# Performance work log

Hardware: AMD Instinct MI355X
Metric: run time of the kernel (lower is better)

The kernel has to match this reference:

```python
import jax, jax.numpy as jnp
import numpy as np
from jax import lax

INPLANES = 512
PLANES = 512
MID = PLANES // 4  # expansion = 4
G = 4              # patch_groups
EPS = 1e-5


def _conv(x, w, groups, pad):
    return lax.conv_general_dilated(
        x, w, window_strides=(1, 1), padding=[(pad, pad), (pad, pad)],
        dimension_numbers=('NCHW', 'OIHW', 'NCHW'), feature_group_count=groups)


def _bn(x, gamma, beta, mean, var):
    scale = gamma / jnp.sqrt(var + EPS)
    return x * scale[None, :, None, None] + (beta - mean * scale)[None, :, None, None]


def _upmask(mask, c, h, w):
    # [b,g,mh,mw] -> repeat each group over c//g channels (group-major channel order),
    # then nearest-upsample to (h, w) (exact integer repeat, matches F.interpolate nearest)
    b, g, mh, mw = mask.shape
    m = jnp.repeat(mask, c // g, axis=1)
    m = jnp.repeat(m, h // mh, axis=2)
    m = jnp.repeat(m, w // mw, axis=3)
    return m


def setup_inputs() -> dict:
    key = jax.random.key(0)
    ks = jax.random.split(key, 20)
    x = jax.random.normal(ks[0], (16, INPLANES, 56, 56), dtype=jnp.float32)
    mask = jax.random.randint(ks[1], (16, G, 7, 7), 0, 2).astype(jnp.float32)
    s = 0.05
    w1 = jax.random.normal(ks[2], (MID, INPLANES // G, 1, 1), dtype=jnp.float32) * s
    w2 = jax.random.normal(ks[3], (MID, MID // G, 3, 3), dtype=jnp.float32) * s
    w3 = jax.random.normal(ks[4], (PLANES, MID // G, 1, 1), dtype=jnp.float32) * s
    def bnp(k, c):
        k1, k2, k3, k4 = jax.random.split(k, 4)
        return (jax.random.normal(k1, (c,), jnp.float32) * 0.1 + 1.0,  # gamma
                jax.random.normal(k2, (c,), jnp.float32) * 0.1,        # beta
                jax.random.normal(k3, (c,), jnp.float32) * 0.1,        # running mean
                jax.random.uniform(k4, (c,), jnp.float32, 0.5, 1.5))   # running var
    g1, b1, m1, v1 = bnp(ks[5], MID)
    g2, b2, m2, v2 = bnp(ks[6], MID)
    g3, b3, m3, v3 = bnp(ks[7], PLANES)
    return dict(x=x, mask=mask, w1=w1, g1=g1, b1=b1, m1=m1, v1=v1,
                w2=w2, g2=g2, b2=b2, m2=m2, v2=v2,
                w3=w3, g3=g3, b3=b3, m3=m3, v3=v3)


def reference(x, mask, w1, g1, b1, m1, v1, w2, g2, b2, m2, v2, w3, g3, b3, m3, v3):
    b, c, h, w = x.shape
    residual = x
    mask1 = _upmask(mask, c, h, w)           # [b, c, h, w]
    out = x * mask1
    out = jax.nn.relu(_bn(_conv(out, w1, G, 0), g1, b1, m1, v1))  # [b, MID, h, w]
    mask2 = _upmask(mask, out.shape[1], h, w)
    out = out * mask2
    out = jax.nn.relu(_bn(_conv(out, w2, G, 1), g2, b2, m2, v2))
    out = out * mask2
    out = _bn(_conv(out, w3, G, 0), g3, b3, m3, v3)
    out = out + residual
    return jax.nn.relu(out)
```

## Files before the change

### kernel.cpp

```cpp
#include <hip/hip_runtime.h>
#include <stdint.h>

typedef unsigned short U16;
typedef unsigned int   U32;
typedef __attribute__((ext_vector_type(8))) short short8;
typedef __attribute__((ext_vector_type(4))) float floatx4;

#define HW 3136

__device__ __forceinline__ U16 f2b(float f){
    union { float f; unsigned int i; } v; v.f = f;
    unsigned int u = (v.i + 0x7FFFu + ((v.i >> 16) & 1u)) >> 16;
    return (U16)u;
}
__device__ __forceinline__ short8 pack8(const float* p){
    float4 a = *reinterpret_cast<const float4*>(p);
    float4 b = *reinterpret_cast<const float4*>(p + 4);
    short8 r;
    r[0]=(short)f2b(a.x); r[1]=(short)f2b(a.y); r[2]=(short)f2b(a.z); r[3]=(short)f2b(a.w);
    r[4]=(short)f2b(b.x); r[5]=(short)f2b(b.y); r[6]=(short)f2b(b.z); r[7]=(short)f2b(b.w);
    return r;
}

__global__ void k_pre(const float* __restrict__ w2,
                      const float* g1, const float* b1, const float* m1, const float* v1,
                      const float* g2, const float* b2, const float* m2, const float* v2,
                      const float* g3, const float* b3, const float* m3, const float* v3,
                      U16* __restrict__ w2t, float* __restrict__ bn){
  int i = blockIdx.x * 256 + threadIdx.x;
  if (i < 4*9*32*32) {
    int ic  = i & 31;
    int oc  = (i >> 5) & 31;
    int gt  = i >> 10;
    int g_  = gt / 9, tap = gt % 9;
    w2t[i] = f2b(w2[((g_*32 + oc)*32 + ic)*9 + tap]);
  } else {
    int j = i - 4*9*32*32;
    if (j >= 768) return;
    const float *gp, *bp, *mp, *vp; int c, so, sho;
    if (j < 128)      { c = j;       gp=g1; bp=b1; mp=m1; vp=v1; so = 0;   sho = 128;  }
    else if (j < 256) { c = j - 128; gp=g2; bp=b2; mp=m2; vp=v2; so = 256; sho = 384;  }
    else              { c = j - 256; gp=g3; bp=b3; mp=m3; vp=v3; so = 512; sho = 1024; }
    float s = gp[c] / sqrtf(vp[c] + 1e-5f);
    bn[so + c]  = s;
    bn[sho + c] = bp[c] - mp[c] * s;
  }
}

__global__ __launch_bounds__(512) void k_conv1(const float* __restrict__ x,
        const float* __restrict__ mask, const float* __restrict__ w1,
        const float* __restrict__ bn, U16* __restrict__ t1){
  const int t = threadIdx.x;
  const int lane = t & 63, wave = t >> 6;
  const int quad = lane >> 4, l15 = lane & 15;
  const int oct = wave & 1, pxq = wave >> 1;
  const int b = blockIdx.z, g = blockIdx.y, mh = blockIdx.x;
  const int h0 = mh*8, wbase = pxq*112;
  __shared__ float mk[7];
  __shared__ __align__(16) U16 xs[32*456];
  if (t < 7) mk[t] = mask[((b*4 + g)*7 + mh)*7 + t];
  const float* xg = x + (size_t)(b*512 + g*128)*HW + h0*56;
  U16* t1g = t1 + (size_t)(b*128 + g*32)*HW + h0*56;

  const float* wg = w1 + (size_t)(g*32)*128;
  short8 afr[4];
  #pragma unroll
  for (int ks = 0; ks < 4; ++ks)
    afr[ks] = pack8(wg + (oct*16 + l15)*128 + ks*32 + quad*8);

  floatx4 acc[7] = {};
  #pragma unroll
  for (int ch = 0; ch < 4; ++ch){
    __syncthreads();
    #pragma unroll
    for (int k = 0; k < 7; ++k){
      int idx = k*512 + t;
      int ic = idx / 112, f = idx - ic*112;
      int px = f*4;
      float4 v = *reinterpret_cast<const float4*>(xg + (size_t)(ch*32 + ic)*HW + px);
      float m = mk[(px % 56) >> 3];
      U32 lo = (U32)f2b(v.x*m) | ((U32)f2b(v.y*m) << 16);
      U32 hi = (U32)f2b(v.z*m) | ((U32)f2b(v.w*m) << 16);
      *reinterpret_cast<uint2*>(&xs[ic*456 + px]) = make_uint2(lo, hi);
    }
    __syncthreads();
    #pragma unroll
    for (int pxt = 0; pxt < 7; ++pxt){
      short8 bfr;
      #pragma unroll
      for (int j = 0; j < 8; ++j)
        bfr[j] = (short)xs[(quad*8 + j)*456 + wbase + pxt*16 + l15];
      acc[pxt] = __builtin_amdgcn_mfma_f32_16x16x32_bf16(afr[ch], bfr, acc[pxt], 0,0,0);
    }
  }
  #pragma unroll
  for (int reg = 0; reg < 4; ++reg){
    int oc = oct*16 + quad*4 + reg;
    float sc = bn[g*32 + oc], sh = bn[128 + g*32 + oc];
    #pragma unroll
    for (int pxt = 0; pxt < 7; ++pxt){
      int px = wbase + pxt*16 + l15;
      float y = fmaxf(sc*acc[pxt][reg] + sh, 0.0f) * mk[(px % 56) >> 3];
      t1g[(size_t)oc*HW + px] = f2b(y);
    }
  }
}

__global__ __launch_bounds__(512) void k_conv23(const U16* __restrict__ t1,
        const float* __restrict__ mask, const U16* __restrict__ w2t,
        const float* __restrict__ w3, const float* __restrict__ bn,
        const float* __restrict__ x, float* __restrict__ out){
  const int t = threadIdx.x;
  const int lane = t & 63, wave = t >> 6;
  const int quad = lane >> 4, l15 = lane & 15;
  const int b = blockIdx.z, g = blockIdx.y, mh = blockIdx.x;
  const int h0 = mh*8;
  __shared__ float mk[7];
  __shared__ __align__(16) U16 s[32*720];
  __shared__ __align__(16) U16 t2s[32*456];
  if (t < 7) mk[t] = mask[((b*4 + g)*7 + mh)*7 + t];
  if (t < 320){
    int ic = t / 10, r = t - ic*10;
    s[(ic*10 + r)*72 + 7]  = 0;
    s[(ic*10 + r)*72 + 64] = 0;
  }
  const U16* tg = t1 + (size_t)(b*128 + g*32)*HW;
  #pragma unroll
  for (int k = 0; k < 5; ++k){
    int idx = k*512 + t;
    if (idx < 2240){
      int ic = idx / 70, rem = idx - ic*70;
      int r = rem / 7, seg = rem - r*7;
      int hh = h0 - 1 + r;
      uint4 v = make_uint4(0,0,0,0);
      if (hh >= 0 && hh < 56)
        v = *reinterpret_cast<const uint4*>(tg + (size_t)ic*HW + hh*56 + seg*8);
      *reinterpret_cast<uint4*>(&s[(ic*10 + r)*72 + 8 + seg*8]) = v;
    }
  }
  __syncthreads();

  {
    const int oct = wave & 1, rq = wave >> 1;
    const U16* wg = w2t + g*9*32*32;
    floatx4 acc[7] = {};
    #pragma unroll
    for (int kh = 0; kh < 3; ++kh){
      const int lr = rq*2 + (l15 >> 3) + kh;
      #pragma unroll
      for (int kw = 0; kw < 3; ++kw){
        int tap = kh*3 + kw;
        short8 a0 = *reinterpret_cast<const short8*>(wg + (tap*32 + oct*16 + l15)*32 + quad*8);
        #pragma unroll
        for (int pxt = 0; pxt < 7; ++pxt){
          int lc = 7 + pxt*8 + (l15 & 7) + kw;
          short8 bfr;
          #pragma unroll
          for (int j = 0; j < 8; ++j)
            bfr[j] = (short)s[((quad*8 + j)*10 + lr)*72 + lc];
          acc[pxt] = __builtin_amdgcn_mfma_f32_16x16x32_bf16(a0, bfr, acc[pxt], 0,0,0);
        }
      }
    }
    const int pr = rq*2 + (l15 >> 3);
    #pragma unroll
    for (int reg = 0; reg < 4; ++reg){
      int oc = oct*16 + quad*4 + reg;
      float sc = bn[256 + g*32 + oc], sh = bn[384 + g*32 + oc];
      #pragma unroll
      for (int pxt = 0; pxt < 7; ++pxt){
        float y = fmaxf(sc*acc[pxt][reg] + sh, 0.0f) * mk[pxt];
        t2s[oc*456 + pr*56 + pxt*8 + (l15 & 7)] = f2b(y);
      }
    }
  }
  __syncthreads();

  {
    short8 afr = pack8(w3 + (size_t)(g*128 + wave*16 + l15)*32 + quad*8);
    const float* scp = bn + 512 + g*128 + wave*16 + quad*4;
    const float* shp = bn + 1024 + g*128 + wave*16 + quad*4;
    const float* xg = x + (size_t)(b*512 + g*128)*HW + h0*56;
    float* og = out + (size_t)(b*512 + g*128)*HW + h0*56;
    #pragma unroll
    for (int tt = 0; tt < 28; ++tt){
      short8 bfr;
      #pragma unroll
      for (int j = 0; j < 8; ++j)
        bfr[j] = (short)t2s[(quad*8 + j)*456 + tt*16 + l15];
      floatx4 acc = {};
      acc = __builtin_amdgcn_mfma_f32_16x16x32_bf16(afr, bfr, acc, 0,0,0);
      int px = tt*16 + l15;
      #pragma unroll
      for (int reg = 0; reg < 4; ++reg){
        size_t o2 = (size_t)(wave*16 + quad*4 + reg)*HW + px;
        og[o2] = fmaxf(scp[reg]*acc[reg] + shp[reg] + xg[o2], 0.0f);
      }
    }
  }
}

extern "C" void kernel_launch(void* const* d_in, const int* in_sizes, int n_in,
                              void* d_out, int out_size, void* d_ws, size_t ws_size,
                              hipStream_t stream){
  const float* x    = (const float*)d_in[0];
  const float* mask = (const float*)d_in[1];
  const float* w1   = (const float*)d_in[2];
  const float* g1   = (const float*)d_in[3];
  const float* b1   = (const float*)d_in[4];
  const float* m1   = (const float*)d_in[5];
  const float* v1   = (const float*)d_in[6];
  const float* w2   = (const float*)d_in[7];
  const float* g2   = (const float*)d_in[8];
  const float* b2   = (const float*)d_in[9];
  const float* m2   = (const float*)d_in[10];
  const float* v2   = (const float*)d_in[11];
  const float* w3   = (const float*)d_in[12];
  const float* g3   = (const float*)d_in[13];
  const float* b3   = (const float*)d_in[14];
  const float* m3   = (const float*)d_in[15];
  const float* v3   = (const float*)d_in[16];

  char* ws = (char*)d_ws;
  U16*   w2t = (U16*)ws;
  float* bn  = (float*)(ws + 73728);
  U16*   t1  = (U16*)(ws + 79872);

  k_pre<<<147, 256, 0, stream>>>(w2, g1,b1,m1,v1, g2,b2,m2,v2, g3,b3,m3,v3, w2t, bn);
  dim3 grid(7, 4, 16);
  k_conv1<<<grid, 512, 0, stream>>>(x, mask, w1, bn, t1);
  k_conv23<<<grid, 512, 0, stream>>>(t1, mask, w2t, w3, bn, x, (float*)d_out);
}
```

Measured before the change: 287.0 us.

## Store intermediates channel-last so MFMA B-fragments load as single vectors

Changes the intermediate t1 from channel-major to pixel-major [b,g,px,32] layout and rearranges the conv2 and conv3 LDS tiles with 32 channels contiguous per pixel (padded stride 40). The B operand of each MFMA can then be read as one 16-byte vector instead of eight scalar LDS loads. The conv2 input buffer is reused for the t2 tile, which needs an extra barrier but lowers LDS use. The conv1 LDS row stride is padded from 456 to 460 to reduce bank conflicts, and the conv1 epilogue writes 4 packed channels per store.

```diff
diff --git a/kernel.cpp b/kernel.cpp
--- a/kernel.cpp
+++ b/kernel.cpp
@@ -7,6 +7,7 @@
 typedef __attribute__((ext_vector_type(4))) float floatx4;
 
 #define HW 3136
+#define ICS 40
 
 __device__ __forceinline__ U16 f2b(float f){
     union { float f; unsigned int i; } v; v.f = f;
@@ -57,10 +58,10 @@
   const int b = blockIdx.z, g = blockIdx.y, mh = blockIdx.x;
   const int h0 = mh*8, wbase = pxq*112;
   __shared__ float mk[7];
-  __shared__ __align__(16) U16 xs[32*456];
+  __shared__ __align__(16) U16 xs[32*460];
   if (t < 7) mk[t] = mask[((b*4 + g)*7 + mh)*7 + t];
   const float* xg = x + (size_t)(b*512 + g*128)*HW + h0*56;
-  U16* t1g = t1 + (size_t)(b*128 + g*32)*HW + h0*56;
+  U16* t1g = t1 + ((size_t)(b*4 + g)*HW + h0*56)*32;
 
   const float* wg = w1 + (size_t)(g*32)*128;
   short8 afr[4];
@@ -81,7 +82,7 @@
       float m = mk[(px % 56) >> 3];
       U32 lo = (U32)f2b(v.x*m) | ((U32)f2b(v.y*m) << 16);
       U32 hi = (U32)f2b(v.z*m) | ((U32)f2b(v.w*m) << 16);
-      *reinterpret_cast<uint2*>(&xs[ic*456 + px]) = make_uint2(lo, hi);
+      *reinterpret_cast<uint2*>(&xs[ic*460 + px]) = make_uint2(lo, hi);
     }
     __syncthreads();
     #pragma unroll
@@ -89,20 +90,22 @@
       short8 bfr;
       #pragma unroll
       for (int j = 0; j < 8; ++j)
-        bfr[j] = (short)xs[(quad*8 + j)*456 + wbase + pxt*16 + l15];
+        bfr[j] = (short)xs[(quad*8 + j)*460 + wbase + pxt*16 + l15];
       acc[pxt] = __builtin_amdgcn_mfma_f32_16x16x32_bf16(afr[ch], bfr, acc[pxt], 0,0,0);
     }
   }
-  #pragma unroll
-  for (int reg = 0; reg < 4; ++reg){
-    int oc = oct*16 + quad*4 + reg;
-    float sc = bn[g*32 + oc], sh = bn[128 + g*32 + oc];
-    #pragma unroll
-    for (int pxt = 0; pxt < 7; ++pxt){
-      int px = wbase + pxt*16 + l15;
-      float y = fmaxf(sc*acc[pxt][reg] + sh, 0.0f) * mk[(px % 56) >> 3];
-      t1g[(size_t)oc*HW + px] = f2b(y);
-    }
+  const float* scp = bn + g*32 + oct*16 + quad*4;
+  const float* shp = scp + 128;
+  #pragma unroll
+  for (int pxt = 0; pxt < 7; ++pxt){
+    int px = wbase + pxt*16 + l15;
+    float m = mk[(px % 56) >> 3];
+    U16 y[4];
+    #pragma unroll
+    for (int reg = 0; reg < 4; ++reg)
+      y[reg] = f2b(fmaxf(scp[reg]*acc[pxt][reg] + shp[reg], 0.0f) * m);
+    *reinterpret_cast<uint2*>(t1g + (size_t)px*32 + oct*16 + quad*4) =
+        make_uint2((U32)y[0] | ((U32)y[1]<<16), (U32)y[2] | ((U32)y[3]<<16));
   }
 }
 
@@ -116,34 +119,35 @@
   const int b = blockIdx.z, g = blockIdx.y, mh = blockIdx.x;
   const int h0 = mh*8;
   __shared__ float mk[7];
-  __shared__ __align__(16) U16 s[32*720];
-  __shared__ __align__(16) U16 t2s[32*456];
+  __shared__ __align__(16) U16 s[580*ICS];
+  U16* t2s = s;
   if (t < 7) mk[t] = mask[((b*4 + g)*7 + mh)*7 + t];
-  if (t < 320){
-    int ic = t / 10, r = t - ic*10;
-    s[(ic*10 + r)*72 + 7]  = 0;
-    s[(ic*10 + r)*72 + 64] = 0;
-  }
-  const U16* tg = t1 + (size_t)(b*128 + g*32)*HW;
+  if (t < 80){
+    int si = t >> 2, part = t & 3;
+    int r = si >> 1, side = si & 1;
+    *reinterpret_cast<uint4*>(&s[(r*58 + (side ? 57 : 0))*ICS + part*8]) =
+        make_uint4(0,0,0,0);
+  }
+  const U16* tg = t1 + (size_t)(b*4 + g)*HW*32;
   #pragma unroll
   for (int k = 0; k < 5; ++k){
     int idx = k*512 + t;
     if (idx < 2240){
-      int ic = idx / 70, rem = idx - ic*70;
-      int r = rem / 7, seg = rem - r*7;
+      int part = idx & 3, pxi = idx >> 2;
+      int r = pxi / 56, c = pxi - r*56;
       int hh = h0 - 1 + r;
       uint4 v = make_uint4(0,0,0,0);
-      if (hh >= 0 && hh < 56)
-        v = *reinterpret_cast<const uint4*>(tg + (size_t)ic*HW + hh*56 + seg*8);
-      *reinterpret_cast<uint4*>(&s[(ic*10 + r)*72 + 8 + seg*8]) = v;
+      if ((unsigned)hh < 56u)
+        v = *reinterpret_cast<const uint4*>(tg + (size_t)(hh*56 + c)*32 + part*8);
+      *reinterpret_cast<uint4*>(&s[(r*58 + c + 1)*ICS + part*8]) = v;
     }
   }
   __syncthreads();
 
+  const int oct = wave & 1, rq = wave >> 1;
+  floatx4 acc[7] = {};
   {
-    const int oct = wave & 1, rq = wave >> 1;
     const U16* wg = w2t + g*9*32*32;
-    floatx4 acc[7] = {};
     #pragma unroll
     for (int kh = 0; kh < 3; ++kh){
       const int lr = rq*2 + (l15 >> 3) + kh;
@@ -153,25 +157,30 @@
         short8 a0 = *reinterpret_cast<const short8*>(wg + (tap*32 + oct*16 + l15)*32 + quad*8);
         #pragma unroll
         for (int pxt = 0; pxt < 7; ++pxt){
-          int lc = 7 + pxt*8 + (l15 & 7) + kw;
-          short8 bfr;
-          #pragma unroll
-          for (int j = 0; j < 8; ++j)
-            bfr[j] = (short)s[((quad*8 + j)*10 + lr)*72 + lc];
+          int cslot = pxt*8 + (l15 & 7) + kw;
+          short8 bfr = *reinterpret_cast<const short8*>(
+              &s[(lr*58 + cslot)*ICS + quad*8]);
           acc[pxt] = __builtin_amdgcn_mfma_f32_16x16x32_bf16(a0, bfr, acc[pxt], 0,0,0);
         }
       }
     }
+  }
+  __syncthreads();
+
+  {
     const int pr = rq*2 + (l15 >> 3);
-    #pragma unroll
-    for (int reg = 0; reg < 4; ++reg){
-      int oc = oct*16 + quad*4 + reg;
-      float sc = bn[256 + g*32 + oc], sh = bn[384 + g*32 + oc];
-      #pragma unroll
-      for (int pxt = 0; pxt < 7; ++pxt){
-        float y = fmaxf(sc*acc[pxt][reg] + sh, 0.0f) * mk[pxt];
-        t2s[oc*456 + pr*56 + pxt*8 + (l15 & 7)] = f2b(y);
-      }
+    const float* scp = bn + 256 + g*32 + oct*16 + quad*4;
+    const float* shp = bn + 384 + g*32 + oct*16 + quad*4;
+    #pragma unroll
+    for (int pxt = 0; pxt < 7; ++pxt){
+      float m = mk[pxt];
+      U16 y[4];
+      #pragma unroll
+      for (int reg = 0; reg < 4; ++reg)
+        y[reg] = f2b(fmaxf(scp[reg]*acc[pxt][reg] + shp[reg], 0.0f) * m);
+      int px = pr*56 + pxt*8 + (l15 & 7);
+      *reinterpret_cast<uint2*>(&t2s[px*ICS + oct*16 + quad*4]) =
+          make_uint2((U32)y[0] | ((U32)y[1]<<16), (U32)y[2] | ((U32)y[3]<<16));
     }
   }
   __syncthreads();
@@ -184,17 +193,14 @@
     float* og = out + (size_t)(b*512 + g*128)*HW + h0*56;
     #pragma unroll
     for (int tt = 0; tt < 28; ++tt){
-      short8 bfr;
-      #pragma unroll
-      for (int j = 0; j < 8; ++j)
-        bfr[j] = (short)t2s[(quad*8 + j)*456 + tt*16 + l15];
-      floatx4 acc = {};
-      acc = __builtin_amdgcn_mfma_f32_16x16x32_bf16(afr, bfr, acc, 0,0,0);
       int px = tt*16 + l15;
+      short8 bfr = *reinterpret_cast<const short8*>(&t2s[px*ICS + quad*8]);
+      floatx4 acc3 = {};
+      acc3 = __builtin_amdgcn_mfma_f32_16x16x32_bf16(afr, bfr, acc3, 0,0,0);
       #pragma unroll
       for (int reg = 0; reg < 4; ++reg){
         size_t o2 = (size_t)(wave*16 + quad*4 + reg)*HW + px;
-        og[o2] = fmaxf(scp[reg]*acc[reg] + shp[reg] + xg[o2], 0.0f);
+        og[o2] = fmaxf(scp[reg]*acc3[reg] + shp[reg] + xg[o2], 0.0f);
       }
     }
   }
```

New measurement: 275.8 us. -3.9%, faster.
